# Optimization experiments

Measured on AMD Instinct MI355X. Metric: run time of the kernel, lower is better.

The kernel has to match this reference:

```python
import jax, jax.numpy as jnp
import numpy as np

N_NODES = 50000
N_EDGES = 800000
IN_DIM = 64
HID_DIM = 64
OUT_DIM = 16
N_RELS = 16
N_BASES = 4


def setup_inputs() -> dict:
    key = jax.random.key(0)
    ks = jax.random.split(key, 11)
    feats = jax.random.normal(ks[0], (N_NODES, IN_DIM), dtype=jnp.float32)
    src = jax.random.randint(ks[1], (N_EDGES,), 0, N_NODES, dtype=jnp.int32)
    dst = jax.random.randint(ks[2], (N_EDGES,), 0, N_NODES, dtype=jnp.int32)
    edge_type = jax.random.randint(ks[3], (N_EDGES,), 0, N_RELS, dtype=jnp.int32)
    edge_norm = jax.random.uniform(ks[4], (N_EDGES,), dtype=jnp.float32)
    # basis-decomposed relation weights: W[r] = sum_b coef[r,b] * bases[b]
    bases1 = jax.random.normal(ks[5], (N_BASES, IN_DIM, HID_DIM), dtype=jnp.float32) * (1.0 / np.sqrt(IN_DIM))
    coef1 = jax.random.normal(ks[6], (N_RELS, N_BASES), dtype=jnp.float32)
    bias1 = jnp.zeros((HID_DIM,), dtype=jnp.float32)
    bases2 = jax.random.normal(ks[7], (N_BASES, HID_DIM, OUT_DIM), dtype=jnp.float32) * (1.0 / np.sqrt(HID_DIM))
    coef2 = jax.random.normal(ks[8], (N_RELS, N_BASES), dtype=jnp.float32)
    bias2 = jnp.zeros((OUT_DIM,), dtype=jnp.float32)
    return {"feats": feats, "src": src, "dst": dst, "edge_type": edge_type,
            "edge_norm": edge_norm, "bases1": bases1, "coef1": coef1, "bias1": bias1,
            "bases2": bases2, "coef2": coef2, "bias2": bias2}


def _rel_graph_conv(x, src, dst, edge_type, edge_norm, bases, coef, bias):
    """One RelGraphConv layer (basis decomposition, low-mem: gather coef, not W)."""
    xs = x[src]                                   # [E, in]  gather source feats
    t = jnp.einsum('ei,bio->ebo', xs, bases)      # [E, B, out] per-basis transform
    c = coef[edge_type]                            # [E, B]   per-edge relation coefs
    msg = jnp.einsum('eb,ebo->eo', c, t)          # [E, out]
    msg = msg * edge_norm[:, None]                # apply edge norm
    h = jax.ops.segment_sum(msg, dst, num_segments=N_NODES)  # scatter-add by dst
    return jax.nn.relu(h + bias)                  # bias + activation (dropout=0, eval)


def reference(feats, src, dst, edge_type, edge_norm, bases1, coef1, bias1, bases2, coef2, bias2):
    h = _rel_graph_conv(feats, src, dst, edge_type, edge_norm, bases1, coef1, bias1)
    h = _rel_graph_conv(h, src, dst, edge_type, edge_norm, bases2, coef2, bias2)
    return h
```

## Files before the change

### kernel.cpp

```cpp
#include <hip/hip_runtime.h>

#define N_NODES 50000
#define N_EDGES 800000

typedef __attribute__((ext_vector_type(8))) short bf16x8;
typedef __attribute__((ext_vector_type(4))) float f32x4;

__device__ __forceinline__ unsigned bf16rne(float x) {
  unsigned u = __float_as_uint(x);
  return (u + 0x7FFFu + ((u >> 16) & 1u)) >> 16;
}
__device__ __forceinline__ unsigned packbf2(float a, float b) {
  return bf16rne(a) | (bf16rne(b) << 16);
}
__device__ __forceinline__ float bflo(unsigned u) { return __uint_as_float(u << 16); }
__device__ __forceinline__ float bfhi(unsigned u) { return __uint_as_float(u & 0xFFFF0000u); }

__global__ __launch_bounds__(256) void k_prep_hist(
    const float4* __restrict__ feats4, uint2* __restrict__ xbf,
    const float* __restrict__ bases1, const float* __restrict__ bases2,
    unsigned short* __restrict__ b1T, unsigned short* __restrict__ b2p,
    const int* __restrict__ dst, int* __restrict__ deg,
    int* __restrict__ rank) {
  if (blockIdx.x < 3125) {
    const int i = blockIdx.x * 256 + threadIdx.x;
    float4 v = feats4[i];
    xbf[i] = make_uint2(packbf2(v.x, v.y), packbf2(v.z, v.w));
    rank[i] = atomicAdd(&deg[dst[i]], 1);
  } else {
    for (int idx = threadIdx.x; idx < 64 * 256; idx += 256) {
      int o = idx >> 8, q = idx & 255;
      b1T[idx] = (unsigned short)bf16rne(bases1[q * 64 + o]);
    }
    for (int idx = threadIdx.x; idx < 64 * 64; idx += 256) {
      int j = idx >> 6, k = idx & 63;
      int o = j >> 2, b = j & 3;
      b2p[idx] = (unsigned short)bf16rne(bases2[b * 1024 + k * 16 + o]);
    }
  }
}

__global__ __launch_bounds__(1024) void k_scan1(const int* __restrict__ deg,
                                                int* __restrict__ rowp,
                                                int* __restrict__ bsum) {
  __shared__ int wsum[16];
  const int tid = threadIdx.x, lane = tid & 63, wid = tid >> 6;
  const int i = blockIdx.x * 1024 + tid;
  int v = (i < N_NODES) ? deg[i] : 0;
  int incl = v;
#pragma unroll
  for (int off = 1; off < 64; off <<= 1) {
    int t = __shfl_up(incl, off, 64);
    if (lane >= off) incl += t;
  }
  if (lane == 63) wsum[wid] = incl;
  __syncthreads();
  if (tid < 16) {
    int wi = wsum[tid];
#pragma unroll
    for (int off = 1; off < 16; off <<= 1) {
      int t = __shfl_up(wi, off, 64);
      if (lane >= off) wi += t;
    }
    wsum[tid] = wi;
  }
  __syncthreads();
  int woff = (wid > 0) ? wsum[wid - 1] : 0;
  int incl_all = incl + woff;
  if (i < N_NODES) rowp[i + 1] = incl_all;
  if (tid == 1023) bsum[blockIdx.x] = incl_all;
}

__global__ __launch_bounds__(1024) void k_scan3(int* __restrict__ rowp,
                                                const int* __restrict__ bsum,
                                                int nblk) {
  __shared__ int s_off;
  const int tid = threadIdx.x;
  if (tid < 64) {
    int v = (tid < nblk && tid < blockIdx.x) ? bsum[tid] : 0;
#pragma unroll
    for (int off = 32; off >= 1; off >>= 1) v += __shfl_down(v, off, 64);
    if (tid == 0) s_off = v;
  }
  __syncthreads();
  const int i = blockIdx.x * 1024 + tid;
  if (i < N_NODES) rowp[i + 1] += s_off;
  if (i == 0) rowp[0] = 0;
}

__global__ __launch_bounds__(256) void k_scatter(
    const int* __restrict__ src, const int* __restrict__ dst,
    const int* __restrict__ ety, const float* __restrict__ enorm,
    const int* __restrict__ rowp, const int* __restrict__ rank,
    uint2* __restrict__ s_edge) {
  int e = blockIdx.x * 256 + threadIdx.x;
  if (e >= N_EDGES) return;
  const int pos = rowp[dst[e]] + rank[e];
  s_edge[pos] = make_uint2((unsigned)src[e] | ((unsigned)ety[e] << 16),
                           __float_as_uint(enorm[e]));
}

#define ROWB 264
__device__ __forceinline__ void gather_node(
    const int* __restrict__ rowp, const uint2* __restrict__ s_edge,
    const uint2* __restrict__ xv, const float4* __restrict__ coefLDS,
    unsigned short* __restrict__ uA, int node, int m, int lane) {
  const int eslot = lane >> 4, ch4 = lane & 15;
  const int beg = rowp[node], end = rowp[node + 1];
  float4 a0 = {0, 0, 0, 0}, a1 = {0, 0, 0, 0}, a2 = {0, 0, 0, 0}, a3 = {0, 0, 0, 0};
  int j = beg + eslot;
  uint2 rec0 = {0, 0}, rec1 = {0, 0}, xp = {0, 0};
  if (j < end) rec0 = s_edge[j];
  if (j + 4 < end) rec1 = s_edge[j + 4];
  if (j < end) xp = xv[(rec0.x & 0xFFFF) * 16 + ch4];
  while (j < end) {
    uint2 rec2 = {0, 0}, xp1 = {0, 0};
    if (j + 8 < end) rec2 = s_edge[j + 8];
    if (j + 4 < end) xp1 = xv[(rec1.x & 0xFFFF) * 16 + ch4];
    const float nm = __uint_as_float(rec0.y);
    const float4 c = coefLDS[rec0.x >> 16];
    const float w0 = nm * c.x, w1 = nm * c.y, w2 = nm * c.z, w3 = nm * c.w;
    const float x0 = bflo(xp.x), x1 = bfhi(xp.x), x2 = bflo(xp.y), x3 = bfhi(xp.y);
    a0.x += w0 * x0; a0.y += w0 * x1; a0.z += w0 * x2; a0.w += w0 * x3;
    a1.x += w1 * x0; a1.y += w1 * x1; a1.z += w1 * x2; a1.w += w1 * x3;
    a2.x += w2 * x0; a2.y += w2 * x1; a2.z += w2 * x2; a2.w += w2 * x3;
    a3.x += w3 * x0; a3.y += w3 * x1; a3.z += w3 * x2; a3.w += w3 * x3;
    j += 4; rec0 = rec1; rec1 = rec2; xp = xp1;
  }
#define RED1(x) x += __shfl_down(x, 32, 64); x += __shfl_down(x, 16, 64)
  RED1(a0.x); RED1(a0.y); RED1(a0.z); RED1(a0.w);
  RED1(a1.x); RED1(a1.y); RED1(a1.z); RED1(a1.w);
  RED1(a2.x); RED1(a2.y); RED1(a2.z); RED1(a2.w);
  RED1(a3.x); RED1(a3.y); RED1(a3.z); RED1(a3.w);
#undef RED1
  if (eslot == 0) {
    unsigned short* row = uA + m * ROWB + 4 * ch4;
    *(uint2*)(row + 0 * 64) = make_uint2(packbf2(a0.x, a0.y), packbf2(a0.z, a0.w));
    *(uint2*)(row + 1 * 64) = make_uint2(packbf2(a1.x, a1.y), packbf2(a1.z, a1.w));
    *(uint2*)(row + 2 * 64) = make_uint2(packbf2(a2.x, a2.y), packbf2(a2.z, a2.w));
    *(uint2*)(row + 3 * 64) = make_uint2(packbf2(a3.x, a3.y), packbf2(a3.z, a3.w));
  }
}

__global__ __launch_bounds__(256) void k_l1_fused(
    const int* __restrict__ rowp, const uint2* __restrict__ s_edge,
    const uint2* __restrict__ xbf, const float* __restrict__ coef1,
    const unsigned short* __restrict__ b1T,
    const float* __restrict__ bias1,
    const unsigned short* __restrict__ b2p,
    uint2* __restrict__ y2bf) {
  __shared__ __align__(16) unsigned short uA[16 * ROWB];
  __shared__ float coefs[64];
  __shared__ float cmat[16 * 68];
  const int wid = threadIdx.x >> 6, lane = threadIdx.x & 63;
  if (threadIdx.x < 64) coefs[threadIdx.x] = coef1[threadIdx.x];
  __syncthreads();
  const int nbase = blockIdx.x * 16;
#pragma unroll
  for (int jn = 0; jn < 4; ++jn) {
    const int m = wid * 4 + jn;
    gather_node(rowp, s_edge, xbf, (const float4*)coefs, uA, nbase + m, m, lane);
  }
  __syncthreads();
  const int nloc = lane & 15, kgrp = lane >> 4;
  f32x4 acc = {0.f, 0.f, 0.f, 0.f};
#pragma unroll
  for (int ks = 0; ks < 8; ++ks) {
    const int k0 = ks * 32 + kgrp * 8;
    const bf16x8 a = *(const bf16x8*)&uA[nloc * ROWB + k0];
    const bf16x8 b = *(const bf16x8*)&b1T[(wid * 16 + nloc) * 256 + k0];
    acc = __builtin_amdgcn_mfma_f32_16x16x32_bf16(a, b, acc, 0, 0, 0);
  }
  {
    const int o = wid * 16 + nloc;
    const float bs = bias1[o];
#pragma unroll
    for (int r = 0; r < 4; ++r) {
      const int m = (lane >> 4) * 4 + r;
      cmat[m * 68 + o] = fmaxf(acc[r] + bs, 0.f);
    }
  }
  __syncthreads();
  f32x4 acc2 = {0.f, 0.f, 0.f, 0.f};
#pragma unroll
  for (int ks = 0; ks < 2; ++ks) {
    const int k0 = ks * 32 + kgrp * 8;
    const float4 c0 = *(const float4*)&cmat[nloc * 68 + k0];
    const float4 c1 = *(const float4*)&cmat[nloc * 68 + k0 + 4];
    union { bf16x8 v; unsigned u[4]; } au;
    au.u[0] = packbf2(c0.x, c0.y); au.u[1] = packbf2(c0.z, c0.w);
    au.u[2] = packbf2(c1.x, c1.y); au.u[3] = packbf2(c1.z, c1.w);
    const bf16x8 b = *(const bf16x8*)&b2p[(wid * 16 + nloc) * 64 + k0];
    acc2 = __builtin_amdgcn_mfma_f32_16x16x32_bf16(au.v, b, acc2, 0, 0, 0);
  }
  __syncthreads();
#pragma unroll
  for (int r = 0; r < 4; ++r) {
    const int m = (lane >> 4) * 4 + r;
    cmat[m * 68 + wid * 16 + nloc] = acc2[r];
  }
  __syncthreads();
  const int nl = threadIdx.x >> 4, c4 = threadIdx.x & 15;
  const float* cr = &cmat[nl * 68 + 4 * c4];
  y2bf[(size_t)(nbase + nl) * 16 + c4] =
      make_uint2(packbf2(cr[0], cr[1]), packbf2(cr[2], cr[3]));
}

__global__ __launch_bounds__(256) void k_l2_gather(
    const int* __restrict__ rowp, const uint2* __restrict__ s_edge,
    const uint2* __restrict__ y2bf, const float* __restrict__ coef2,
    const float* __restrict__ bias2, float* __restrict__ out) {
  __shared__ float coefs[64];
  if (threadIdx.x < 64) coefs[threadIdx.x] = coef2[threadIdx.x];
  __syncthreads();
  const float4* coefv = (const float4*)coefs;
  const int node = blockIdx.x * 4 + (threadIdx.x >> 6);
  const int lane = threadIdx.x & 63;
  const int eslot = lane >> 4, o = lane & 15;
  const int beg = rowp[node], end = rowp[node + 1];
  float acc = 0.f;
  int j = beg + eslot;
  uint2 rec0 = {0, 0}, rec1 = {0, 0}, yp = {0, 0};
  if (j < end) rec0 = s_edge[j];
  if (j + 4 < end) rec1 = s_edge[j + 4];
  if (j < end) yp = y2bf[(rec0.x & 0xFFFF) * 16 + o];
  while (j < end) {
    uint2 rec2 = {0, 0}, yp1 = {0, 0};
    if (j + 8 < end) rec2 = s_edge[j + 8];
    if (j + 4 < end) yp1 = y2bf[(rec1.x & 0xFFFF) * 16 + o];
    const float nm = __uint_as_float(rec0.y);
    const float4 c = coefv[rec0.x >> 16];
    acc += nm * (c.x * bflo(yp.x) + c.y * bfhi(yp.x) +
                 c.z * bflo(yp.y) + c.w * bfhi(yp.y));
    j += 4; rec0 = rec1; rec1 = rec2; yp = yp1;
  }
  acc += __shfl_down(acc, 32, 64);
  acc += __shfl_down(acc, 16, 64);
  if (eslot == 0) out[(size_t)node * 16 + o] = fmaxf(acc + bias2[o], 0.f);
}

extern "C" void kernel_launch(void* const* d_in, const int* in_sizes, int n_in,
                              void* d_out, int out_size, void* d_ws, size_t ws_size,
                              hipStream_t stream) {
  const float* feats  = (const float*)d_in[0];
  const int*   src    = (const int*)d_in[1];
  const int*   dst    = (const int*)d_in[2];
  const int*   etype  = (const int*)d_in[3];
  const float* enorm  = (const float*)d_in[4];
  const float* bases1 = (const float*)d_in[5];
  const float* coef1  = (const float*)d_in[6];
  const float* bias1  = (const float*)d_in[7];
  const float* bases2 = (const float*)d_in[8];
  const float* coef2  = (const float*)d_in[9];
  const float* bias2  = (const float*)d_in[10];

  uint2* xbf    = (uint2*)d_ws;
  uint2* y2bf   = xbf + (size_t)N_NODES * 16;
  uint2* s_edge = y2bf + (size_t)N_NODES * 16;
  int*   rank   = (int*)(s_edge + N_EDGES);
  unsigned short* b1T = (unsigned short*)(rank + N_EDGES);
  unsigned short* b2p = b1T + 64 * 256;
  int*   deg    = (int*)(b2p + 64 * 64);
  int*   rowp   = deg + N_NODES;
  int*   bsum   = rowp + N_NODES + 1;

  const int SCAN_BLKS = (N_NODES + 1023) / 1024;

  hipMemsetAsync(deg, 0, N_NODES * sizeof(int), stream);

  k_prep_hist<<<3126, 256, 0, stream>>>((const float4*)feats, xbf, bases1,
                                        bases2, b1T, b2p, dst, deg, rank);
  k_scan1<<<SCAN_BLKS, 1024, 0, stream>>>(deg, rowp, bsum);
  k_scan3<<<SCAN_BLKS, 1024, 0, stream>>>(rowp, bsum, SCAN_BLKS);
  k_scatter<<<N_EDGES / 256, 256, 0, stream>>>(src, dst, etype, enorm,
                                               rowp, rank, s_edge);
  k_l1_fused<<<N_NODES / 16, 256, 0, stream>>>(rowp, s_edge, xbf, coef1,
                                               b1T, bias1, b2p, y2bf);
  k_l2_gather<<<N_NODES / 4, 256, 0, stream>>>(rowp, s_edge, y2bf, coef2,
                                               bias2, (float*)d_out);
}
```

Baseline: 213.7 us.

## Interleave per-wave node gathers and widen layer-2 gather to 16-byte loads

In the layer-1 fused kernel, each wave now walks the edge lists of its four nodes at the same time instead of one after another, so more independent gather loads are in flight to hide memory latency. This costs many more live registers (64 accumulators plus per-node pipeline state) and may lower occupancy. The layer-2 gather kernel now reads 8 bf16 values per lane as uint4 loads with 8 edge slots per node, handles two nodes per wave, and writes float2 outputs, which halves the number of blocks.

Measured after the change: 229.7 us. 7.5% more time.

```diff
diff --git a/kernel.cpp b/kernel.cpp
--- a/kernel.cpp
+++ b/kernel.cpp
@@ -101,47 +101,6 @@
 }
 
 #define ROWB 264
-__device__ __forceinline__ void gather_node(
-    const int* __restrict__ rowp, const uint2* __restrict__ s_edge,
-    const uint2* __restrict__ xv, const float4* __restrict__ coefLDS,
-    unsigned short* __restrict__ uA, int node, int m, int lane) {
-  const int eslot = lane >> 4, ch4 = lane & 15;
-  const int beg = rowp[node], end = rowp[node + 1];
-  float4 a0 = {0, 0, 0, 0}, a1 = {0, 0, 0, 0}, a2 = {0, 0, 0, 0}, a3 = {0, 0, 0, 0};
-  int j = beg + eslot;
-  uint2 rec0 = {0, 0}, rec1 = {0, 0}, xp = {0, 0};
-  if (j < end) rec0 = s_edge[j];
-  if (j + 4 < end) rec1 = s_edge[j + 4];
-  if (j < end) xp = xv[(rec0.x & 0xFFFF) * 16 + ch4];
-  while (j < end) {
-    uint2 rec2 = {0, 0}, xp1 = {0, 0};
-    if (j + 8 < end) rec2 = s_edge[j + 8];
-    if (j + 4 < end) xp1 = xv[(rec1.x & 0xFFFF) * 16 + ch4];
-    const float nm = __uint_as_float(rec0.y);
-    const float4 c = coefLDS[rec0.x >> 16];
-    const float w0 = nm * c.x, w1 = nm * c.y, w2 = nm * c.z, w3 = nm * c.w;
-    const float x0 = bflo(xp.x), x1 = bfhi(xp.x), x2 = bflo(xp.y), x3 = bfhi(xp.y);
-    a0.x += w0 * x0; a0.y += w0 * x1; a0.z += w0 * x2; a0.w += w0 * x3;
-    a1.x += w1 * x0; a1.y += w1 * x1; a1.z += w1 * x2; a1.w += w1 * x3;
-    a2.x += w2 * x0; a2.y += w2 * x1; a2.z += w2 * x2; a2.w += w2 * x3;
-    a3.x += w3 * x0; a3.y += w3 * x1; a3.z += w3 * x2; a3.w += w3 * x3;
-    j += 4; rec0 = rec1; rec1 = rec2; xp = xp1;
-  }
-#define RED1(x) x += __shfl_down(x, 32, 64); x += __shfl_down(x, 16, 64)
-  RED1(a0.x); RED1(a0.y); RED1(a0.z); RED1(a0.w);
-  RED1(a1.x); RED1(a1.y); RED1(a1.z); RED1(a1.w);
-  RED1(a2.x); RED1(a2.y); RED1(a2.z); RED1(a2.w);
-  RED1(a3.x); RED1(a3.y); RED1(a3.z); RED1(a3.w);
-#undef RED1
-  if (eslot == 0) {
-    unsigned short* row = uA + m * ROWB + 4 * ch4;
-    *(uint2*)(row + 0 * 64) = make_uint2(packbf2(a0.x, a0.y), packbf2(a0.z, a0.w));
-    *(uint2*)(row + 1 * 64) = make_uint2(packbf2(a1.x, a1.y), packbf2(a1.z, a1.w));
-    *(uint2*)(row + 2 * 64) = make_uint2(packbf2(a2.x, a2.y), packbf2(a2.z, a2.w));
-    *(uint2*)(row + 3 * 64) = make_uint2(packbf2(a3.x, a3.y), packbf2(a3.z, a3.w));
-  }
-}
-
 __global__ __launch_bounds__(256) void k_l1_fused(
     const int* __restrict__ rowp, const uint2* __restrict__ s_edge,
     const uint2* __restrict__ xbf, const float* __restrict__ coef1,
@@ -155,21 +114,80 @@
   const int wid = threadIdx.x >> 6, lane = threadIdx.x & 63;
   if (threadIdx.x < 64) coefs[threadIdx.x] = coef1[threadIdx.x];
   __syncthreads();
+  const float4* coefLDS = (const float4*)coefs;
   const int nbase = blockIdx.x * 16;
-#pragma unroll
-  for (int jn = 0; jn < 4; ++jn) {
-    const int m = wid * 4 + jn;
-    gather_node(rowp, s_edge, xbf, (const float4*)coefs, uA, nbase + m, m, lane);
-  }
-  __syncthreads();
+  const int eslot = lane >> 4, ch4 = lane & 15;
+
+  int j[4], jend[4];
+  float4 acc[4][4];
+  uint2 r0[4], r1[4], xp[4];
+#pragma unroll
+  for (int m = 0; m < 4; ++m) {
+    const int node = nbase + wid * 4 + m;
+    const int beg = rowp[node];
+    jend[m] = rowp[node + 1];
+    j[m] = beg + eslot;
+#pragma unroll
+    for (int b = 0; b < 4; ++b) acc[m][b] = make_float4(0.f, 0.f, 0.f, 0.f);
+    r0[m] = make_uint2(0, 0); r1[m] = make_uint2(0, 0); xp[m] = make_uint2(0, 0);
+    if (j[m] < jend[m]) r0[m] = s_edge[j[m]];
+    if (j[m] + 4 < jend[m]) r1[m] = s_edge[j[m] + 4];
+  }
+#pragma unroll
+  for (int m = 0; m < 4; ++m)
+    if (j[m] < jend[m]) xp[m] = xbf[(r0[m].x & 0xFFFF) * 16 + ch4];
+
+  while ((j[0] < jend[0]) | (j[1] < jend[1]) | (j[2] < jend[2]) |
+         (j[3] < jend[3])) {
+#pragma unroll
+    for (int m = 0; m < 4; ++m) {
+      uint2 r2 = make_uint2(0, 0), xp1 = make_uint2(0, 0);
+      if (j[m] + 8 < jend[m]) r2 = s_edge[j[m] + 8];
+      if (j[m] + 4 < jend[m]) xp1 = xbf[(r1[m].x & 0xFFFF) * 16 + ch4];
+      if (j[m] < jend[m]) {
+        const float nm = __uint_as_float(r0[m].y);
+        const float4 c = coefLDS[r0[m].x >> 16];
+        const float w0 = nm * c.x, w1 = nm * c.y, w2 = nm * c.z, w3 = nm * c.w;
+        const float x0 = bflo(xp[m].x), x1 = bfhi(xp[m].x);
+        const float x2 = bflo(xp[m].y), x3 = bfhi(xp[m].y);
+        acc[m][0].x += w0 * x0; acc[m][0].y += w0 * x1; acc[m][0].z += w0 * x2; acc[m][0].w += w0 * x3;
+        acc[m][1].x += w1 * x0; acc[m][1].y += w1 * x1; acc[m][1].z += w1 * x2; acc[m][1].w += w1 * x3;
+        acc[m][2].x += w2 * x0; acc[m][2].y += w2 * x1; acc[m][2].z += w2 * x2; acc[m][2].w += w2 * x3;
+        acc[m][3].x += w3 * x0; acc[m][3].y += w3 * x1; acc[m][3].z += w3 * x2; acc[m][3].w += w3 * x3;
+      }
+      j[m] += 4; r0[m] = r1[m]; r1[m] = r2; xp[m] = xp1;
+    }
+  }
+#pragma unroll
+  for (int m = 0; m < 4; ++m) {
+#define RED1(x) x += __shfl_down(x, 32, 64); x += __shfl_down(x, 16, 64)
+    RED1(acc[m][0].x); RED1(acc[m][0].y); RED1(acc[m][0].z); RED1(acc[m][0].w);
+    RED1(acc[m][1].x); RED1(acc[m][1].y); RED1(acc[m][1].z); RED1(acc[m][1].w);
+    RED1(acc[m][2].x); RED1(acc[m][2].y); RED1(acc[m][2].z); RED1(acc[m][2].w);
+    RED1(acc[m][3].x); RED1(acc[m][3].y); RED1(acc[m][3].z); RED1(acc[m][3].w);
+#undef RED1
+    if (eslot == 0) {
+      unsigned short* row = uA + (wid * 4 + m) * ROWB + 4 * ch4;
+      *(uint2*)(row + 0 * 64) = make_uint2(packbf2(acc[m][0].x, acc[m][0].y),
+                                           packbf2(acc[m][0].z, acc[m][0].w));
+      *(uint2*)(row + 1 * 64) = make_uint2(packbf2(acc[m][1].x, acc[m][1].y),
+                                           packbf2(acc[m][1].z, acc[m][1].w));
+      *(uint2*)(row + 2 * 64) = make_uint2(packbf2(acc[m][2].x, acc[m][2].y),
+                                           packbf2(acc[m][2].z, acc[m][2].w));
+      *(uint2*)(row + 3 * 64) = make_uint2(packbf2(acc[m][3].x, acc[m][3].y),
+                                           packbf2(acc[m][3].z, acc[m][3].w));
+    }
+  }
+  __syncthreads();
+
   const int nloc = lane & 15, kgrp = lane >> 4;
-  f32x4 acc = {0.f, 0.f, 0.f, 0.f};
+  f32x4 acc1 = {0.f, 0.f, 0.f, 0.f};
 #pragma unroll
   for (int ks = 0; ks < 8; ++ks) {
     const int k0 = ks * 32 + kgrp * 8;
     const bf16x8 a = *(const bf16x8*)&uA[nloc * ROWB + k0];
     const bf16x8 b = *(const bf16x8*)&b1T[(wid * 16 + nloc) * 256 + k0];
-    acc = __builtin_amdgcn_mfma_f32_16x16x32_bf16(a, b, acc, 0, 0, 0);
+    acc1 = __builtin_amdgcn_mfma_f32_16x16x32_bf16(a, b, acc1, 0, 0, 0);
   }
   {
     const int o = wid * 16 + nloc;
@@ -177,7 +195,7 @@
 #pragma unroll
     for (int r = 0; r < 4; ++r) {
       const int m = (lane >> 4) * 4 + r;
-      cmat[m * 68 + o] = fmaxf(acc[r] + bs, 0.f);
+      cmat[m * 68 + o] = fmaxf(acc1[r] + bs, 0.f);
     }
   }
   __syncthreads();
@@ -208,35 +226,71 @@
 
 __global__ __launch_bounds__(256) void k_l2_gather(
     const int* __restrict__ rowp, const uint2* __restrict__ s_edge,
-    const uint2* __restrict__ y2bf, const float* __restrict__ coef2,
-    const float* __restrict__ bias2, float* __restrict__ out) {
+    const uint4* __restrict__ y2v,
+    const float* __restrict__ coef2, const float* __restrict__ bias2,
+    float2* __restrict__ out) {
   __shared__ float coefs[64];
   if (threadIdx.x < 64) coefs[threadIdx.x] = coef2[threadIdx.x];
   __syncthreads();
   const float4* coefv = (const float4*)coefs;
-  const int node = blockIdx.x * 4 + (threadIdx.x >> 6);
-  const int lane = threadIdx.x & 63;
-  const int eslot = lane >> 4, o = lane & 15;
-  const int beg = rowp[node], end = rowp[node + 1];
-  float acc = 0.f;
-  int j = beg + eslot;
-  uint2 rec0 = {0, 0}, rec1 = {0, 0}, yp = {0, 0};
-  if (j < end) rec0 = s_edge[j];
-  if (j + 4 < end) rec1 = s_edge[j + 4];
-  if (j < end) yp = y2bf[(rec0.x & 0xFFFF) * 16 + o];
-  while (j < end) {
-    uint2 rec2 = {0, 0}, yp1 = {0, 0};
-    if (j + 8 < end) rec2 = s_edge[j + 8];
-    if (j + 4 < end) yp1 = y2bf[(rec1.x & 0xFFFF) * 16 + o];
-    const float nm = __uint_as_float(rec0.y);
-    const float4 c = coefv[rec0.x >> 16];
-    acc += nm * (c.x * bflo(yp.x) + c.y * bfhi(yp.x) +
-                 c.z * bflo(yp.y) + c.w * bfhi(yp.y));
-    j += 4; rec0 = rec1; rec1 = rec2; yp = yp1;
-  }
-  acc += __shfl_down(acc, 32, 64);
-  acc += __shfl_down(acc, 16, 64);
-  if (eslot == 0) out[(size_t)node * 16 + o] = fmaxf(acc + bias2[o], 0.f);
+  const int wid = threadIdx.x >> 6, lane = threadIdx.x & 63;
+  const int eslot = lane >> 3, og = lane & 7;
+  const int nbase = blockIdx.x * 8 + wid * 2;
+
+  int j[2], jend[2];
+  float a0[2] = {0.f, 0.f}, a1[2] = {0.f, 0.f};
+  uint2 r0[2], r1[2];
+  uint4 yp[2];
+#pragma unroll
+  for (int m = 0; m < 2; ++m) {
+    const int node = nbase + m;
+    const int beg = rowp[node];
+    jend[m] = rowp[node + 1];
+    j[m] = beg + eslot;
+    r0[m] = make_uint2(0, 0); r1[m] = make_uint2(0, 0);
+    yp[m] = make_uint4(0, 0, 0, 0);
+    if (j[m] < jend[m]) r0[m] = s_edge[j[m]];
+    if (j[m] + 8 < jend[m]) r1[m] = s_edge[j[m] + 8];
+  }
+#pragma unroll
+  for (int m = 0; m < 2; ++m)
+    if (j[m] < jend[m]) yp[m] = y2v[(r0[m].x & 0xFFFF) * 8 + og];
+
+  while ((j[0] < jend[0]) | (j[1] < jend[1])) {
+#pragma unroll
+    for (int m = 0; m < 2; ++m) {
+      uint2 r2 = make_uint2(0, 0);
+      uint4 yp1 = make_uint4(0, 0, 0, 0);
+      if (j[m] + 16 < jend[m]) r2 = s_edge[j[m] + 16];
+      if (j[m] + 8 < jend[m]) yp1 = y2v[(r1[m].x & 0xFFFF) * 8 + og];
+      if (j[m] < jend[m]) {
+        const float nm = __uint_as_float(r0[m].y);
+        const float4 c = coefv[r0[m].x >> 16];
+        a0[m] += nm * (c.x * bflo(yp[m].x) + c.y * bfhi(yp[m].x) +
+                       c.z * bflo(yp[m].y) + c.w * bfhi(yp[m].y));
+        a1[m] += nm * (c.x * bflo(yp[m].z) + c.y * bfhi(yp[m].z) +
+                       c.z * bflo(yp[m].w) + c.w * bfhi(yp[m].w));
+      }
+      j[m] += 8; r0[m] = r1[m]; r1[m] = r2; yp[m] = yp1;
+    }
+  }
+#pragma unroll
+  for (int m = 0; m < 2; ++m) {
+    a0[m] += __shfl_down(a0[m], 32, 64);
+    a0[m] += __shfl_down(a0[m], 16, 64);
+    a0[m] += __shfl_down(a0[m], 8, 64);
+    a1[m] += __shfl_down(a1[m], 32, 64);
+    a1[m] += __shfl_down(a1[m], 16, 64);
+    a1[m] += __shfl_down(a1[m], 8, 64);
+  }
+  if (eslot == 0) {
+    const float b0 = bias2[2 * og], b1 = bias2[2 * og + 1];
+#pragma unroll
+    for (int m = 0; m < 2; ++m) {
+      out[(size_t)(nbase + m) * 8 + og] =
+          make_float2(fmaxf(a0[m] + b0, 0.f), fmaxf(a1[m] + b1, 0.f));
+    }
+  }
 }
 
 extern "C" void kernel_launch(void* const* d_in, const int* in_sizes, int n_in,
@@ -276,6 +330,7 @@
                                                rowp, rank, s_edge);
   k_l1_fused<<<N_NODES / 16, 256, 0, stream>>>(rowp, s_edge, xbf, coef1,
                                                b1T, bias1, b2p, y2bf);
-  k_l2_gather<<<N_NODES / 4, 256, 0, stream>>>(rowp, s_edge, y2bf, coef2,
-                                               bias2, (float*)d_out);
-}
+  k_l2_gather<<<N_NODES / 8, 256, 0, stream>>>(rowp, s_edge,
+                                               (const uint4*)y2bf, coef2,
+                                               bias2, (float2*)d_out);
+}
```
